# Performance work log

Measured on AMD Instinct MI355X. Metric: run time of the kernel, lower is better.

The kernel has to match this reference:

```python
import jax, jax.numpy as jnp
import numpy as np

B = 8192
H_IN = 128
H = 512
Z = 128
N = 512   # must equal H due to W_up(h,h) -> W_down(n,.) chaining in the source
RW = 16
TEMP = 0.666
EPS = 1e-20


def _xavier(key, shape):
    fan_in, fan_out = shape[0], shape[1]
    lim = float(np.sqrt(6.0 / (fan_in + fan_out)))
    return jax.random.uniform(key, shape, jnp.float32, -lim, lim)


def setup_inputs() -> dict:
    key = jax.random.key(0)
    ks = jax.random.split(key, 24)
    inp = {
        'latent': jax.random.normal(ks[0], (B, Z), jnp.float32),
        'inputs': jnp.zeros((B, H_IN), jnp.float32),
        'gumbel_u': jax.random.uniform(ks[1], (RW, B, N), jnp.float32),
        # weights stored [in, out] for x @ W
        'W_int': _xavier(ks[2], (Z, H)),   'b_int': jnp.zeros((H,), jnp.float32),
        'W_intl': _xavier(ks[3], (Z, H)),  'b_intl': jnp.zeros((H,), jnp.float32),
        'W_hup': _xavier(ks[4], (H, H)),   'b_hup': jnp.zeros((H,), jnp.float32),
        'W_cup': _xavier(ks[5], (H, H)),   'b_cup': jnp.zeros((H,), jnp.float32),
        'W_hupl': _xavier(ks[6], (H, H)),  'b_hupl': jnp.zeros((H,), jnp.float32),
        'W_cupl': _xavier(ks[7], (H, H)),  'b_cupl': jnp.zeros((H,), jnp.float32),
        'W_lstm': _xavier(ks[8], (H_IN + H, 4 * H)), 'b_lstm': jnp.zeros((4 * H,), jnp.float32),
        'W_up': _xavier(ks[9], (H, H)),    'b_up': jnp.zeros((H,), jnp.float32),
        'W_down': _xavier(ks[10], (N, H_IN)),        # no bias
        'W_downl': _xavier(ks[11], (N, H_IN)),       # no bias
        'W_outl': _xavier(ks[12], (H, 1)), 'b_outl': jnp.zeros((1,), jnp.float32),
    }
    return inp


def _lstm_step(x, hx, cx, W_lstm, b_lstm):
    gates = jnp.concatenate([x, hx], axis=1) @ W_lstm + b_lstm  # [B, 4H]
    i, g, f, o = jnp.split(gates, 4, axis=1)
    cy = cx * jax.nn.sigmoid(f + 1.0) + jax.nn.sigmoid(i) * jnp.tanh(g)
    hy = jax.nn.sigmoid(o) * jnp.tanh(cy)
    return hy, cy


def _forward(latent, inputs, gumbel_u,
             W_int, b_int, W_intl, b_intl,
             W_hup, b_hup, W_cup, b_cup,
             W_hupl, b_hupl, W_cupl, b_cupl,
             W_lstm, b_lstm, W_up, b_up,
             W_down, W_downl, W_outl, b_outl):
    inter = jnp.tanh(latent @ W_int + b_int)
    hx = jnp.tanh(inter @ W_hup + b_hup)
    cx = jnp.tanh(inter @ W_cup + b_cup)
    inter_l = jnp.tanh(latent @ W_intl + b_intl)
    hxl = jnp.tanh(inter_l @ W_hupl + b_hupl)
    cxl = jnp.tanh(inter_l @ W_cupl + b_cupl)

    def step1(carry, u):
        x, h, c = carry
        hy, cy = _lstm_step(x, h, c, W_lstm, b_lstm)
        logits = hy @ W_up + b_up                       # [B, N]
        g = -jnp.log(-jnp.log(u + EPS) + EPS)           # gumbel noise
        y = jax.nn.softmax((logits + g) / TEMP, axis=1)
        y_hard = (y == jnp.max(y, axis=1, keepdims=True)).astype(y.dtype)
        y = jax.lax.stop_gradient(y_hard - y) + y       # straight-through hard sample
        return (y @ W_down, hy, cy), y

    _, out_steps = jax.lax.scan(step1, (inputs, hx, cx), gumbel_u)  # [RW, B, N]

    def step2(carry, y):
        h, c = carry
        xl = y @ W_downl
        hy, cy = _lstm_step(xl, h, c, W_lstm, b_lstm)   # source reuses lstm_cell here
        return (hy, cy), hy @ W_outl + b_outl           # [B, 1]

    _, line_steps = jax.lax.scan(step2, (hxl, cxl), out_steps)      # [RW, B, 1]

    return (jnp.transpose(out_steps, (1, 0, 2)),   # [B, RW, N]
            jnp.transpose(line_steps, (1, 0, 2)))  # [B, RW, 1]


def reference(latent, inputs, gumbel_u,
              W_int, b_int, W_intl, b_intl,
              W_hup, b_hup, W_cup, b_cup,
              W_hupl, b_hupl, W_cupl, b_cupl,
              W_lstm, b_lstm, W_up, b_up,
              W_down, W_downl, W_outl, b_outl):
    return _forward(latent, inputs, gumbel_u,
                    W_int, b_int, W_intl, b_intl,
                    W_hup, b_hup, W_cup, b_cup,
                    W_hupl, b_hupl, W_cupl, b_cupl,
                    W_lstm, b_lstm, W_up, b_up,
                    W_down, W_downl, W_outl, b_outl)
```

## Files before the change

kernel.cpp:

```cpp
#include <hip/hip_runtime.h>

#define NB 8192
#define NH 512
#define NZ 128
#define NIN 128
#define NN 512
#define NRW 16
#define NG 2048

typedef _Float16 f16;
typedef _Float16 f16x8 __attribute__((ext_vector_type(8)));
typedef float f32x4 __attribute__((ext_vector_type(4)));

#define LO_SCALE 2048.0f
#define LO_INV   (1.0f / 2048.0f)

__device__ __forceinline__ float sigm(float x) { return 1.0f / (1.0f + expf(-x)); }

__device__ __forceinline__ int oc_of(int c)
{
    return (((c >> 4) & 3) << 9) + ((c >> 6) << 4) + (c & 15);
}
__device__ __forceinline__ int cperm(int j)
{
    return (j & 15) | (((j >> 4) & 31) << 6) | (((j >> 9) & 3) << 4);
}

__device__ __forceinline__ void swz_xcd(int& bx, int& by)
{
    const int gx = gridDim.x;
    const int nwg = gx * gridDim.y;
    int lin = by * gx + bx;
    lin = (lin & 7) * (nwg >> 3) + (lin >> 3);
    const int sh = 31 - __clz(gx);
    bx = lin & (gx - 1);
    by = lin >> sh;
}

__device__ __forceinline__ void gload16(const f16* g, f16* l)
{
    __builtin_amdgcn_global_load_lds(
        (const __attribute__((address_space(1))) void*)g,
        (__attribute__((address_space(3))) void*)l, 16, 0, 0);
}

__device__ __forceinline__ int swz4(int row) { return (row & 3) ^ ((row >> 2) & 3); }

__device__ __forceinline__ void stage_tile(f16* tilebase, const f16* src,
                                           int rowbase, int K, int kb,
                                           int wid, int lane)
{
#pragma unroll
    for (int q = 0; q < 2; ++q) {
        const int iw = wid * 2 + q;
        const int chunk = (iw << 6) | lane;
        const int row = chunk >> 2;
        const int p = (chunk & 3) ^ swz4(row);
        const f16* g = src + (size_t)(rowbase + row) * K + kb + (p << 3);
        gload16(g, tilebase + (iw << 9));
    }
}

__device__ __forceinline__ f16x8 frag(const f16* tile, int row, int sl)
{
    return *(const f16x8*)(tile + row * 32 + ((sl ^ swz4(row)) << 3));
}

__device__ __forceinline__ void gemm_core(const f16* Ahi, const f16* Alo,
                                          const f16* Bhi, const f16* Blo,
                                          f16 (*sT)[4][128 * 32],
                                          int bm, int bn, int K,
                                          int wid, int lane, int wr, int wc,
                                          f32x4 (&accA)[4][4], f32x4 (&accB)[4][4])
{
    const int NT = K >> 5;
    stage_tile(sT[0][0], Ahi, bm, K, 0, wid, lane);
    stage_tile(sT[0][1], Alo, bm, K, 0, wid, lane);
    __builtin_amdgcn_sched_barrier(0);
    stage_tile(sT[0][2], Bhi, bn, K, 0, wid, lane);
    __builtin_amdgcn_sched_barrier(0);
    stage_tile(sT[0][3], Blo, bn, K, 0, wid, lane);

    const int r16 = lane & 15, sl = lane >> 4;

    for (int kt = 0; kt < NT; ++kt) {
        const int cur = kt & 1;
        const int nxt = cur ^ 1;
        const bool more = (kt + 1 < NT);
        const int kb = (kt + 1) << 5;

        asm volatile("s_waitcnt vmcnt(2)" ::: "memory");
        __builtin_amdgcn_s_barrier();
        __builtin_amdgcn_sched_barrier(0);
        if (more) {
            stage_tile(sT[nxt][0], Ahi, bm, K, kb, wid, lane);
            stage_tile(sT[nxt][1], Alo, bm, K, kb, wid, lane);
        }
        f16x8 ah[4], bh[4];
#pragma unroll
        for (int f = 0; f < 4; ++f) {
            ah[f] = frag(sT[cur][0], wr + f * 16 + r16, sl);
            bh[f] = frag(sT[cur][2], wc + f * 16 + r16, sl);
        }
        __builtin_amdgcn_s_setprio(1);
#pragma unroll
        for (int i = 0; i < 4; ++i)
#pragma unroll
            for (int j = 0; j < 4; ++j)
                accA[i][j] = __builtin_amdgcn_mfma_f32_16x16x32_f16(ah[i], bh[j], accA[i][j], 0, 0, 0);
        __builtin_amdgcn_s_setprio(0);

        __builtin_amdgcn_s_barrier();
        __builtin_amdgcn_sched_barrier(0);
        if (more) stage_tile(sT[nxt][2], Bhi, bn, K, kb, wid, lane);
        f16x8 al[4];
#pragma unroll
        for (int f = 0; f < 4; ++f) al[f] = frag(sT[cur][1], wr + f * 16 + r16, sl);
        __builtin_amdgcn_s_setprio(1);
#pragma unroll
        for (int i = 0; i < 4; ++i)
#pragma unroll
            for (int j = 0; j < 4; ++j)
                accB[i][j] = __builtin_amdgcn_mfma_f32_16x16x32_f16(al[i], bh[j], accB[i][j], 0, 0, 0);
        __builtin_amdgcn_s_setprio(0);

        if (more) asm volatile("s_waitcnt vmcnt(6)" ::: "memory");
        else      asm volatile("s_waitcnt vmcnt(0)" ::: "memory");
        __builtin_amdgcn_s_barrier();
        __builtin_amdgcn_sched_barrier(0);
        if (more) stage_tile(sT[nxt][3], Blo, bn, K, kb, wid, lane);
        f16x8 bl[4];
#pragma unroll
        for (int f = 0; f < 4; ++f) bl[f] = frag(sT[cur][3], wc + f * 16 + r16, sl);
        __builtin_amdgcn_s_setprio(1);
#pragma unroll
        for (int i = 0; i < 4; ++i)
#pragma unroll
            for (int j = 0; j < 4; ++j)
                accB[i][j] = __builtin_amdgcn_mfma_f32_16x16x32_f16(ah[i], bl[j], accB[i][j], 0, 0, 0);
        __builtin_amdgcn_s_setprio(0);
    }
}

__device__ __forceinline__ void gemm_core1(const f16* Ahi, const f16* Bhi,
                                           f16 (*sT)[2][128 * 32],
                                           int bm, int bn, int K,
                                           int wid, int lane, int wr, int wc,
                                           f32x4 (&acc)[4][4])
{
    const int NT = K >> 5;
    stage_tile(sT[0][0], Ahi, bm, K, 0, wid, lane);
    stage_tile(sT[0][1], Bhi, bn, K, 0, wid, lane);

    const int r16 = lane & 15, sl = lane >> 4;

    for (int kt = 0; kt < NT; ++kt) {
        const int cur = kt & 1;
        const int nxt = cur ^ 1;
        __syncthreads();
        if (kt + 1 < NT) {
            const int kb = (kt + 1) << 5;
            stage_tile(sT[nxt][0], Ahi, bm, K, kb, wid, lane);
            stage_tile(sT[nxt][1], Bhi, bn, K, kb, wid, lane);
        }
        f16x8 ah[4], bh[4];
#pragma unroll
        for (int f = 0; f < 4; ++f) {
            ah[f] = frag(sT[cur][0], wr + f * 16 + r16, sl);
            bh[f] = frag(sT[cur][1], wc + f * 16 + r16, sl);
        }
        __builtin_amdgcn_s_setprio(1);
#pragma unroll
        for (int i = 0; i < 4; ++i)
#pragma unroll
            for (int j = 0; j < 4; ++j)
                acc[i][j] = __builtin_amdgcn_mfma_f32_16x16x32_f16(ah[i], bh[j], acc[i][j], 0, 0, 0);
        __builtin_amdgcn_s_setprio(0);
    }
}

template<int OUT>
__global__ __launch_bounds__(256, 2)
void mfma_gemm(const f16* __restrict__ Ahi, const f16* __restrict__ Alo,
               const f16* __restrict__ Bhi, const f16* __restrict__ Blo,
               const float* __restrict__ bias,
               float* __restrict__ C, f16* __restrict__ Ohi, f16* __restrict__ Olo,
               int N, int K)
{
    __shared__ f16 sT[2][4][128 * 32];
    int bx = blockIdx.x, by = blockIdx.y;
    swz_xcd(bx, by);
    const int bm = by << 7;
    const int bn = bx << 7;
    const int tid = threadIdx.x;
    const int wid = tid >> 6, lane = tid & 63;
    const int wr = ((wid >> 1) & 1) << 6;
    const int wc = (wid & 1) << 6;

    f32x4 accA[4][4], accB[4][4];
#pragma unroll
    for (int i = 0; i < 4; ++i)
#pragma unroll
        for (int j = 0; j < 4; ++j) { accA[i][j] = (f32x4)(0.0f); accB[i][j] = (f32x4)(0.0f); }

    gemm_core(Ahi, Alo, Bhi, Blo, sT, bm, bn, K, wid, lane, wr, wc, accA, accB);

    const int r16 = lane & 15;
    const int rg = lane >> 4;
#pragma unroll
    for (int i = 0; i < 4; ++i) {
#pragma unroll
        for (int r = 0; r < 4; ++r) {
            const int row = bm + wr + i * 16 + rg * 4 + r;
#pragma unroll
            for (int j = 0; j < 4; ++j) {
                const int col = bn + wc + j * 16 + r16;
                float v = accA[i][j][r] + accB[i][j][r] * LO_INV;
                if (bias) v += bias[col];
                if (OUT >= 1) v = tanhf(v);
                const size_t idx = (size_t)row * N + col;
                if (OUT <= 1) C[idx] = v;
                else {
                    const f16 a = (f16)v;
                    Ohi[idx] = a;
                    if (OUT == 2) Olo[idx] = (f16)((v - (float)a) * LO_SCALE);
                }
            }
        }
    }
}

__global__ __launch_bounds__(256, 2)
void mfma_logits_argmax(const f16* __restrict__ Ahi, const f16* __restrict__ Alo,
                        const f16* __restrict__ Bhi, const f16* __restrict__ Blo,
                        const float* __restrict__ bias,
                        const float* __restrict__ gu,
                        float2* __restrict__ part, int t)
{
    __shared__ f16 sT[2][4][128 * 32];
    int bx = blockIdx.x, by = blockIdx.y;
    swz_xcd(bx, by);
    const int bm = by << 7;
    const int bn = bx << 7;
    const int tid = threadIdx.x;
    const int wid = tid >> 6, lane = tid & 63;
    const int wr = ((wid >> 1) & 1) << 6;
    const int wc = (wid & 1) << 6;

    f32x4 accA[4][4], accB[4][4];
#pragma unroll
    for (int i = 0; i < 4; ++i)
#pragma unroll
        for (int j = 0; j < 4; ++j) { accA[i][j] = (f32x4)(0.0f); accB[i][j] = (f32x4)(0.0f); }

    gemm_core(Ahi, Alo, Bhi, Blo, sT, bm, bn, NN, wid, lane, wr, wc, accA, accB);

    const int r16 = lane & 15;
    const int rg = lane >> 4;
    const int cb = bx * 2 + (wc >> 6);
    float bi[4];
#pragma unroll
    for (int j = 0; j < 4; ++j) bi[j] = bias[bn + wc + j * 16 + r16];

#pragma unroll
    for (int i = 0; i < 4; ++i) {
#pragma unroll
        for (int r = 0; r < 4; ++r) {
            const int row = bm + wr + i * 16 + rg * 4 + r;
            const float* urow = gu + ((size_t)t * NB + row) * NN;
            float best = -INFINITY;
            int bidx = 0x7fffffff;
#pragma unroll
            for (int j = 0; j < 4; ++j) {
                const int col = bn + wc + j * 16 + r16;
                const float u = urow[col];
                const float g = -logf(-logf(u + 1e-20f) + 1e-20f);
                const float v = accA[i][j][r] + accB[i][j][r] * LO_INV + bi[j] + g;
                if (v > best || (v == best && col < bidx)) { best = v; bidx = col; }
            }
#pragma unroll
            for (int msk = 1; msk < 16; msk <<= 1) {
                const float ov = __shfl_xor(best, msk);
                const int oi = __shfl_xor(bidx, msk);
                if (ov > best || (ov == best && oi < bidx)) { best = ov; bidx = oi; }
            }
            if (r16 == 0) part[(size_t)row * 8 + cb] = make_float2(best, (float)bidx);
        }
    }
}

__global__ __launch_bounds__(256)
void finalize_argmax(const float2* __restrict__ part,
                     float* __restrict__ out0, int* __restrict__ kidx, int t)
{
    const int w = threadIdx.x >> 6;
    const int lane = threadIdx.x & 63;
    const int row = blockIdx.x * 4 + w;
    float best = -INFINITY;
    int bi = 0x7fffffff;
    if (lane < 8) {
        const float2 p = part[(size_t)row * 8 + lane];
        best = p.x;
        bi = (int)p.y;
    }
#pragma unroll
    for (int msk = 1; msk < 8; msk <<= 1) {
        const float ov = __shfl_xor(best, msk);
        const int oi = __shfl_xor(bi, msk);
        if (ov > best || (ov == best && oi < bi)) { best = ov; bi = oi; }
    }
    const int win = __shfl(bi, 0);
    if (lane == 0) kidx[(size_t)t * NB + row] = win;
    float* orow = out0 + ((size_t)row * NRW + t) * NN;
    const int c0 = lane * 8;
    float4 v0 = make_float4(c0 == win, c0 + 1 == win, c0 + 2 == win, c0 + 3 == win);
    float4 v1 = make_float4(c0 + 4 == win, c0 + 5 == win, c0 + 6 == win, c0 + 7 == win);
    *(float4*)(orow + c0) = v0;
    *(float4*)(orow + c0 + 4) = v1;
}

template<int HAS_EXTRA>
__global__ __launch_bounds__(256, 2)
void mfma_gate_lstm(const f16* __restrict__ Ahi, const f16* __restrict__ Alo,
                    const f16* __restrict__ Bhi, const f16* __restrict__ Blo,
                    const float* __restrict__ blp,
                    const float* __restrict__ extra, const int* __restrict__ eidx,
                    float* __restrict__ c,
                    f16* __restrict__ h_hi, f16* __restrict__ h_lo)
{
    __shared__ f16 sT[2][4][128 * 32];
    int bx = blockIdx.x, by = blockIdx.y;
    swz_xcd(bx, by);
    const int bm = by << 7;
    const int bn = bx << 7;
    const int tid = threadIdx.x;
    const int wid = tid >> 6, lane = tid & 63;
    const int wr = ((wid >> 1) & 1) << 6;
    const int wc = (wid & 1) << 6;

    f32x4 accA[4][4], accB[4][4];
#pragma unroll
    for (int i = 0; i < 4; ++i)
#pragma unroll
        for (int j = 0; j < 4; ++j) { accA[i][j] = (f32x4)(0.0f); accB[i][j] = (f32x4)(0.0f); }

    gemm_core(Ahi, Alo, Bhi, Blo, sT, bm, bn, NH, wid, lane, wr, wc, accA, accB);

    const int m = lane & 15;
    const int rg = lane >> 4;
    const int colb = bn + wc;
    const int jj = ((colb >> 6) << 4) + m;
    float bi[4];
#pragma unroll
    for (int g = 0; g < 4; ++g) bi[g] = blp[colb + g * 16 + m];

#pragma unroll
    for (int i = 0; i < 4; ++i) {
#pragma unroll
        for (int r = 0; r < 4; ++r) {
            const int row = bm + wr + i * 16 + rg * 4 + r;
            float ex[4] = {0.f, 0.f, 0.f, 0.f};
            if (HAS_EXTRA) {
                const float* exr = extra + (size_t)eidx[row] * NG;
#pragma unroll
                for (int g = 0; g < 4; ++g) ex[g] = exr[colb + g * 16 + m];
            }
            const float ig = accA[i][0][r] + accB[i][0][r] * LO_INV + bi[0] + ex[0];
            const float gg = accA[i][1][r] + accB[i][1][r] * LO_INV + bi[1] + ex[1];
            const float fg = accA[i][2][r] + accB[i][2][r] * LO_INV + bi[2] + ex[2];
            const float og = accA[i][3][r] + accB[i][3][r] * LO_INV + bi[3] + ex[3];
            const size_t cidx = (size_t)row * NH + jj;
            const float cx = c[cidx];
            const float cy = cx * sigm(fg + 1.0f) + sigm(ig) * tanhf(gg);
            const float hy = sigm(og) * tanhf(cy);
            c[cidx] = cy;
            const f16 a = (f16)hy;
            h_hi[cidx] = a;
            h_lo[cidx] = (f16)((hy - (float)a) * LO_SCALE);
        }
    }
}

__global__ __launch_bounds__(256, 2)
void mfma_gate_lstm2(const f16* __restrict__ Ahi, const f16* __restrict__ Bhi,
                     const float* __restrict__ blp,
                     const float* __restrict__ extra, const int* __restrict__ eidx,
                     float* __restrict__ c,
                     f16* __restrict__ h_hi,
                     const float* __restrict__ Woutl,
                     float* __restrict__ out1, int t)
{
    __shared__ f16 sT[2][2][128 * 32];
    int bx = blockIdx.x, by = blockIdx.y;
    swz_xcd(bx, by);
    const int bm = by << 7;
    const int bn = bx << 7;
    const int tid = threadIdx.x;
    const int wid = tid >> 6, lane = tid & 63;
    const int wr = ((wid >> 1) & 1) << 6;
    const int wc = (wid & 1) << 6;

    f32x4 acc[4][4];
#pragma unroll
    for (int i = 0; i < 4; ++i)
#pragma unroll
        for (int j = 0; j < 4; ++j) acc[i][j] = (f32x4)(0.0f);

    gemm_core1(Ahi, Bhi, sT, bm, bn, NH, wid, lane, wr, wc, acc);

    const int m = lane & 15;
    const int rg = lane >> 4;
    const int colb = bn + wc;
    const int jj = ((colb >> 6) << 4) + m;
    const float wout = Woutl[jj];
    float bi[4];
#pragma unroll
    for (int g = 0; g < 4; ++g) bi[g] = blp[colb + g * 16 + m];

#pragma unroll
    for (int i = 0; i < 4; ++i) {
#pragma unroll
        for (int r = 0; r < 4; ++r) {
            const int row = bm + wr + i * 16 + rg * 4 + r;
            const float* exr = extra + (size_t)eidx[row] * NG;
            float ex[4];
#pragma unroll
            for (int g = 0; g < 4; ++g) ex[g] = exr[colb + g * 16 + m];
            const float ig = acc[i][0][r] + bi[0] + ex[0];
            const float gg = acc[i][1][r] + bi[1] + ex[1];
            const float fg = acc[i][2][r] + bi[2] + ex[2];
            const float og = acc[i][3][r] + bi[3] + ex[3];
            const size_t cidx = (size_t)row * NH + jj;
            const float cx = c[cidx];
            const float cy = cx * sigm(fg + 1.0f) + sigm(ig) * tanhf(gg);
            const float hy = sigm(og) * tanhf(cy);
            c[cidx] = cy;
            h_hi[cidx] = (f16)hy;
            float part = hy * wout;
#pragma unroll
            for (int msk = 1; msk < 16; msk <<= 1) part += __shfl_xor(part, msk);
            if (m == 0) atomicAdd(&out1[(size_t)row * NRW + t], part);
        }
    }
}

__global__ __launch_bounds__(256)
void out1_init(float* __restrict__ out1, const float* __restrict__ boutl)
{
    const size_t i = (size_t)blockIdx.x * 256 + threadIdx.x;
    out1[i] = boutl[0];
}

template<int ACT, int PERM>
__global__ __launch_bounds__(256)
void gemm128(const float* __restrict__ A, int lda,
             const float* __restrict__ W, int ldw,
             const float* __restrict__ bias,
             float* __restrict__ C, int ldc, int K)
{
    __shared__ float As[16][128];
    __shared__ float Bs[16][128];
    const int bm = blockIdx.y << 7, bn = blockIdx.x << 7;
    const int tid = threadIdx.x;
    const int tx = tid & 15, ty = tid >> 4;
    const int sar = tid >> 1, sac = (tid & 1) << 3;
    const int sbk = tid >> 4, sbc = (tid & 15) << 3;
    float acc[2][2][4][4] = {};
    const float* Ap = A + (size_t)(bm + sar) * lda + sac;
    const float* Wp = W + (size_t)sbk * ldw + bn + sbc;
    for (int kb = 0; kb < K; kb += 16) {
        const float4 av0 = *(const float4*)(Ap + kb);
        const float4 av1 = *(const float4*)(Ap + kb + 4);
        const float4 bv0 = *(const float4*)(Wp + (size_t)kb * ldw);
        const float4 bv1 = *(const float4*)(Wp + (size_t)kb * ldw + 4);
// ... 19 lines not shown
#pragma unroll
                    for (int i = 0; i < 4; ++i)
#pragma unroll
                        for (int j = 0; j < 4; ++j)
                            acc[rh][ch][i][j] = fmaf(a[rh][i], b[ch][j], acc[rh][ch][i][j]);
        }
    }
    float4 bi4[2] = {make_float4(0.f, 0.f, 0.f, 0.f), make_float4(0.f, 0.f, 0.f, 0.f)};
    if (bias) {
        bi4[0] = *(const float4*)(bias + bn + (tx << 2));
        bi4[1] = *(const float4*)(bias + bn + 64 + (tx << 2));
    }
#pragma unroll
    for (int rh = 0; rh < 2; ++rh)
#pragma unroll
        for (int i = 0; i < 4; ++i) {
            const int row = bm + rh * 64 + (ty << 2) + i;
#pragma unroll
            for (int ch = 0; ch < 2; ++ch) {
                const int col = bn + ch * 64 + (tx << 2);
                float v0 = acc[rh][ch][i][0] + bi4[ch].x;
                float v1 = acc[rh][ch][i][1] + bi4[ch].y;
                float v2 = acc[rh][ch][i][2] + bi4[ch].z;
                float v3 = acc[rh][ch][i][3] + bi4[ch].w;
                if (ACT == 1) { v0 = tanhf(v0); v1 = tanhf(v1); v2 = tanhf(v2); v3 = tanhf(v3); }
                const int wcol = PERM ? cperm(col) : col;
                *(float4*)(C + (size_t)row * ldc + wcol) = make_float4(v0, v1, v2, v3);
            }
        }
}

template<int PERM>
__global__ __launch_bounds__(256)
void tsplit(const float* __restrict__ in, int ldin, int K,
            f16* __restrict__ ohi, f16* __restrict__ olo)
{
    __shared__ float t[32][33];
    const int kb = blockIdx.x << 5, nb = blockIdx.y << 5;
    const int cx = threadIdx.x & 31, ry = threadIdx.x >> 5;
    const int col = PERM ? oc_of(nb + cx) : (nb + cx);
#pragma unroll
    for (int q = 0; q < 4; ++q)
        t[ry + q * 8][cx] = in[(size_t)(kb + ry + q * 8) * ldin + col];
    __syncthreads();
#pragma unroll
    for (int q = 0; q < 4; ++q) {
        const int n = ry + q * 8;
        const float v = t[cx][n];
        const f16 hi = (f16)v;
        ohi[(size_t)(nb + n) * K + kb + cx] = hi;
        if (olo) olo[(size_t)(nb + n) * K + kb + cx] = (f16)((v - (float)hi) * LO_SCALE);
    }
}

__global__ __launch_bounds__(256)
void permb(const float* __restrict__ b, float* __restrict__ bp)
{
    const int c = blockIdx.x * 256 + threadIdx.x;
    bp[c] = b[oc_of(c)];
}

__global__ __launch_bounds__(256)
void split_h(const float* __restrict__ h, f16* __restrict__ hi, f16* __restrict__ lo)
{
    const size_t i = (size_t)blockIdx.x * 256 + threadIdx.x;
    const float v = h[i];
    const f16 a = (f16)v;
    hi[i] = a;
    lo[i] = (f16)((v - (float)a) * LO_SCALE);
}

extern "C" void kernel_launch(void* const* d_in, const int* in_sizes, int n_in,
                              void* d_out, int out_size, void* d_ws, size_t ws_size,
                              hipStream_t stream)
{
    const float* latent  = (const float*)d_in[0];
    const float* gu      = (const float*)d_in[2];
    const float* W_int   = (const float*)d_in[3];
    const float* b_int   = (const float*)d_in[4];
    const float* W_intl  = (const float*)d_in[5];
    const float* b_intl  = (const float*)d_in[6];
    const float* W_hup   = (const float*)d_in[7];
    const float* b_hup   = (const float*)d_in[8];
    const float* W_cup   = (const float*)d_in[9];
    const float* b_cup   = (const float*)d_in[10];
    const float* W_hupl  = (const float*)d_in[11];
    const float* b_hupl  = (const float*)d_in[12];
    const float* W_cupl  = (const float*)d_in[13];
    const float* b_cupl  = (const float*)d_in[14];
    const float* W_lstm  = (const float*)d_in[15];
    const float* b_lstm  = (const float*)d_in[16];
    const float* W_up    = (const float*)d_in[17];
    const float* b_up    = (const float*)d_in[18];
    const float* W_down  = (const float*)d_in[19];
    const float* W_downl = (const float*)d_in[20];
    const float* W_outl  = (const float*)d_in[21];
    const float* b_outl  = (const float*)d_in[22];

    float* out0 = (float*)d_out;
    float* out1 = out0 + (size_t)NB * NRW * NN;

    float* ws     = (float*)d_ws;
    float* c      = ws;
    float* logits = c + (size_t)NB * NH;
    float* gdown  = logits + (size_t)NB * NH;
    float* gdownl = gdown + (size_t)NN * NG;
    float* blp    = gdownl + (size_t)NN * NG;
    float2* part  = (float2*)(blp + NG);
    f16* fp = (f16*)(part + (size_t)NB * 8);
    f16* h_hi[2]; f16* h_lo[2];
    h_hi[0] = fp;                    fp += (size_t)NB * NH;
    h_lo[0] = fp;                    fp += (size_t)NB * NH;
    h_hi[1] = fp;                    fp += (size_t)NB * NH;
    h_lo[1] = fp;                    fp += (size_t)NB * NH;
    f16* i_hi   = fp;                fp += (size_t)NB * NH;
    f16* i_lo   = fp;                fp += (size_t)NB * NH;
    f16* WlT_hi = fp;                fp += (size_t)NG * NH;
    f16* WlT_lo = fp;                fp += (size_t)NG * NH;
    f16* WupT_hi = fp;               fp += (size_t)NN * NH;
    f16* WupT_lo = fp;               fp += (size_t)NN * NH;
    f16* WhT_hi = fp;                fp += (size_t)NH * NH;
    f16* WhT_lo = fp;                fp += (size_t)NH * NH;
    f16* WcT_hi = fp;                fp += (size_t)NH * NH;
    f16* WcT_lo = fp;                fp += (size_t)NH * NH;
    f16* WhlT_hi = fp;               fp += (size_t)NH * NH;
    f16* WhlT_lo = fp;               fp += (size_t)NH * NH;
    f16* WclT_hi = fp;               fp += (size_t)NH * NH;
    f16* WclT_lo = fp;               fp += (size_t)NH * NH;
    int* kidx = (int*)fp;

    const dim3 blk(256);
    const dim3 g_gates(NG / 128, NB / 128);
    const dim3 g_h(NH / 128, NB / 128);
    const dim3 g_pre(NG / 128, NN / 128);
    const dim3 g_sph(NB * NH / 256);

    tsplit<1><<<dim3(NH / 32, NG / 32), blk, 0, stream>>>(W_lstm + (size_t)NIN * NG, NG, NH, WlT_hi, WlT_lo);
    tsplit<0><<<dim3(NH / 32, NN / 32), blk, 0, stream>>>(W_up, NH, NH, WupT_hi, WupT_lo);
    tsplit<0><<<dim3(NH / 32, NH / 32), blk, 0, stream>>>(W_hup, NH, NH, WhT_hi, WhT_lo);
    tsplit<0><<<dim3(NH / 32, NH / 32), blk, 0, stream>>>(W_cup, NH, NH, WcT_hi, WcT_lo);
    tsplit<0><<<dim3(NH / 32, NH / 32), blk, 0, stream>>>(W_hupl, NH, NH, WhlT_hi, WhlT_lo);
    tsplit<0><<<dim3(NH / 32, NH / 32), blk, 0, stream>>>(W_cupl, NH, NH, WclT_hi, WclT_lo);
    permb<<<dim3(NG / 256), blk, 0, stream>>>(b_lstm, blp);
    gemm128<0, 1><<<g_pre, blk, 0, stream>>>(W_down, NIN, W_lstm, NG, nullptr, gdown, NG, NIN);
    gemm128<0, 1><<<g_pre, blk, 0, stream>>>(W_downl, NIN, W_lstm, NG, nullptr, gdownl, NG, NIN);

    gemm128<1, 0><<<g_h, blk, 0, stream>>>(latent, NZ, W_int, NH, b_int, logits, NH, NZ);
    split_h<<<g_sph, blk, 0, stream>>>(logits, i_hi, i_lo);
    mfma_gemm<2><<<g_h, blk, 0, stream>>>(i_hi, i_lo, WhT_hi, WhT_lo, b_hup,
                                          nullptr, h_hi[0], h_lo[0], NH, NH);
    mfma_gemm<1><<<g_h, blk, 0, stream>>>(i_hi, i_lo, WcT_hi, WcT_lo, b_cup,
                                          c, nullptr, nullptr, NH, NH);

    int cur = 0;
    for (int t = 0; t < NRW; ++t) {
        const int nxt = cur ^ 1;
        if (t == 0)
            mfma_gate_lstm<0><<<g_gates, blk, 0, stream>>>(h_hi[cur], h_lo[cur], WlT_hi, WlT_lo,
                                                           blp, nullptr, nullptr,
                                                           c, h_hi[nxt], h_lo[nxt]);
        else
            mfma_gate_lstm<1><<<g_gates, blk, 0, stream>>>(h_hi[cur], h_lo[cur], WlT_hi, WlT_lo,
                                                           blp, gdown, kidx + (size_t)(t - 1) * NB,
                                                           c, h_hi[nxt], h_lo[nxt]);
        mfma_logits_argmax<<<g_h, blk, 0, stream>>>(h_hi[nxt], h_lo[nxt], WupT_hi, WupT_lo,
                                                    b_up, gu, part, t);
        finalize_argmax<<<dim3(NB / 4), blk, 0, stream>>>(part, out0, kidx, t);
        cur = nxt;
    }

    gemm128<1, 0><<<g_h, blk, 0, stream>>>(latent, NZ, W_intl, NH, b_intl, logits, NH, NZ);
    split_h<<<g_sph, blk, 0, stream>>>(logits, i_hi, i_lo);
    mfma_gemm<3><<<g_h, blk, 0, stream>>>(i_hi, i_lo, WhlT_hi, WhlT_lo, b_hupl,
                                          nullptr, h_hi[0], nullptr, NH, NH);
    mfma_gemm<1><<<g_h, blk, 0, stream>>>(i_hi, i_lo, WclT_hi, WclT_lo, b_cupl,
                                          c, nullptr, nullptr, NH, NH);
    out1_init<<<dim3(NB * NRW / 256), blk, 0, stream>>>(out1, b_outl);

    cur = 0;
    for (int t = 0; t < NRW; ++t) {
        const int nxt = cur ^ 1;
        mfma_gate_lstm2<<<g_gates, blk, 0, stream>>>(h_hi[cur], WlT_hi,
                                                     blp, gdownl, kidx + (size_t)t * NB,
                                                     c, h_hi[nxt],
                                                     W_outl, out1, t);
        cur = nxt;
    }
}
```

Measured before the change: 3.088 ms.

## Pre-pack weights into MFMA fragment order and load B directly to registers

Weights are repacked by a new tsplit_pack kernel into per-fragment blocks so each wave loads its B operand straight from global memory into registers, and only the activation tile A is staged through LDS. The three split-precision products now go into a single accumulator without the 2048 lo-scale factor. The per-step finalize_argmax launch is folded into the next gate kernel, which reduces the partial maxima itself. This cuts LDS traffic, barriers and kernel launches per step, but B register loads bypass LDS reuse across waves, and dropping the lo scaling may cost precision through f16 underflow of the residual terms.

```diff
diff --git a/kernel.cpp b/kernel.cpp
--- a/kernel.cpp
+++ b/kernel.cpp
@@ -12,9 +12,6 @@
 typedef _Float16 f16x8 __attribute__((ext_vector_type(8)));
 typedef float f32x4 __attribute__((ext_vector_type(4)));
 
-#define LO_SCALE 2048.0f
-#define LO_INV   (1.0f / 2048.0f)
-
 __device__ __forceinline__ float sigm(float x) { return 1.0f / (1.0f + expf(-x)); }
 
 __device__ __forceinline__ int oc_of(int c)
@@ -47,8 +44,7 @@
 __device__ __forceinline__ int swz4(int row) { return (row & 3) ^ ((row >> 2) & 3); }
 
 __device__ __forceinline__ void stage_tile(f16* tilebase, const f16* src,
-                                           int rowbase, int K, int kb,
-                                           int wid, int lane)
+                                           int rowbase, int kb, int wid, int lane)
 {
 #pragma unroll
     for (int q = 0; q < 2; ++q) {
@@ -56,7 +52,7 @@
         const int chunk = (iw << 6) | lane;
         const int row = chunk >> 2;
         const int p = (chunk & 3) ^ swz4(row);
-        const f16* g = src + (size_t)(rowbase + row) * K + kb + (p << 3);
+        const f16* g = src + (size_t)(rowbase + row) * NH + kb + (p << 3);
         gload16(g, tilebase + (iw << 9));
     }
 }
@@ -66,115 +62,85 @@
     return *(const f16x8*)(tile + row * 32 + ((sl ^ swz4(row)) << 3));
 }
 
-__device__ __forceinline__ void gemm_core(const f16* Ahi, const f16* Alo,
-                                          const f16* Bhi, const f16* Blo,
-                                          f16 (*sT)[4][128 * 32],
-                                          int bm, int bn, int K,
-                                          int wid, int lane, int wr, int wc,
-                                          f32x4 (&accA)[4][4], f32x4 (&accB)[4][4])
-{
-    const int NT = K >> 5;
-    stage_tile(sT[0][0], Ahi, bm, K, 0, wid, lane);
-    stage_tile(sT[0][1], Alo, bm, K, 0, wid, lane);
-    __builtin_amdgcn_sched_barrier(0);
-    stage_tile(sT[0][2], Bhi, bn, K, 0, wid, lane);
-    __builtin_amdgcn_sched_barrier(0);
-    stage_tile(sT[0][3], Blo, bn, K, 0, wid, lane);
-
+__device__ __forceinline__ void readA(f16x8 (&a)[4], const f16* sbuf, int wr, int r16, int sl)
+{
+#pragma unroll
+    for (int f = 0; f < 4; ++f) a[f] = frag(sbuf, wr + f * 16 + r16, sl);
+}
+
+__device__ __forceinline__ void loadBfr(f16x8 (&d)[4], const f16* p, size_t base)
+{
+#pragma unroll
+    for (int f = 0; f < 4; ++f) d[f] = *(const f16x8*)(p + base + f * 512);
+}
+
+__device__ __forceinline__ f32x4 MM(const f16x8 a, const f16x8 b, f32x4 c)
+{
+    return __builtin_amdgcn_mfma_f32_16x16x32_f16(a, b, c, 0, 0, 0);
+}
+
+template<int SPLIT>
+__device__ __forceinline__ void core3(const f16* Ahi, const f16* Alo,
+                                      const f16* Bph, const f16* Bpl,
+                                      f16* s0h, f16* s0l, f16* s1h, f16* s1l,
+                                      int bm, int bnblk, int wid, int lane, int wr, int wc2,
+                                      f32x4 (&acc)[4][4])
+{
     const int r16 = lane & 15, sl = lane >> 4;
-
-    for (int kt = 0; kt < NT; ++kt) {
-        const int cur = kt & 1;
-        const int nxt = cur ^ 1;
-        const bool more = (kt + 1 < NT);
-        const int kb = (kt + 1) << 5;
-
-        asm volatile("s_waitcnt vmcnt(2)" ::: "memory");
-        __builtin_amdgcn_s_barrier();
-        __builtin_amdgcn_sched_barrier(0);
-        if (more) {
-            stage_tile(sT[nxt][0], Ahi, bm, K, kb, wid, lane);
-            stage_tile(sT[nxt][1], Alo, bm, K, kb, wid, lane);
-        }
-        f16x8 ah[4], bh[4];
-#pragma unroll
-        for (int f = 0; f < 4; ++f) {
-            ah[f] = frag(sT[cur][0], wr + f * 16 + r16, sl);
-            bh[f] = frag(sT[cur][2], wc + f * 16 + r16, sl);
-        }
+    const size_t bwoff = (size_t)(wc2 << 11) + lane * 8;
+    f16x8 bAh[4], bAl[4], bBh[4], bBl[4];
+
+    stage_tile(s0h, Ahi, bm, 0, wid, lane);
+    if (SPLIT) stage_tile(s0l, Alo, bm, 0, wid, lane);
+    loadBfr(bAh, Bph, (((size_t)bnblk << 4) << 12) + bwoff);
+    if (SPLIT) loadBfr(bAl, Bpl, (((size_t)bnblk << 4) << 12) + bwoff);
+
+#pragma unroll 1
+    for (int kt = 0; kt < 16; kt += 2) {
+        __syncthreads();
+        {
+            const int kn = kt + 1;
+            stage_tile(s1h, Ahi, bm, kn << 5, wid, lane);
+            if (SPLIT) stage_tile(s1l, Alo, bm, kn << 5, wid, lane);
+            loadBfr(bBh, Bph, ((((size_t)bnblk << 4) + kn) << 12) + bwoff);
+            if (SPLIT) loadBfr(bBl, Bpl, ((((size_t)bnblk << 4) + kn) << 12) + bwoff);
+        }
+        f16x8 ah[4], al[4];
+        readA(ah, s0h, wr, r16, sl);
+        if (SPLIT) readA(al, s0l, wr, r16, sl);
         __builtin_amdgcn_s_setprio(1);
 #pragma unroll
         for (int i = 0; i < 4; ++i)
 #pragma unroll
-            for (int j = 0; j < 4; ++j)
-                accA[i][j] = __builtin_amdgcn_mfma_f32_16x16x32_f16(ah[i], bh[j], accA[i][j], 0, 0, 0);
+            for (int j = 0; j < 4; ++j) {
+                acc[i][j] = MM(ah[i], bAh[j], acc[i][j]);
+                if (SPLIT) {
+                    acc[i][j] = MM(al[i], bAh[j], acc[i][j]);
+                    acc[i][j] = MM(ah[i], bAl[j], acc[i][j]);
+                }
+            }
         __builtin_amdgcn_s_setprio(0);
-
-        __builtin_amdgcn_s_barrier();
-        __builtin_amdgcn_sched_barrier(0);
-        if (more) stage_tile(sT[nxt][2], Bhi, bn, K, kb, wid, lane);
-        f16x8 al[4];
-#pragma unroll
-        for (int f = 0; f < 4; ++f) al[f] = frag(sT[cur][1], wr + f * 16 + r16, sl);
+        __syncthreads();
+        if (kt + 2 < 16) {
+            const int kn = kt + 2;
+            stage_tile(s0h, Ahi, bm, kn << 5, wid, lane);
+            if (SPLIT) stage_tile(s0l, Alo, bm, kn << 5, wid, lane);
+            loadBfr(bAh, Bph, ((((size_t)bnblk << 4) + kn) << 12) + bwoff);
+            if (SPLIT) loadBfr(bAl, Bpl, ((((size_t)bnblk << 4) + kn) << 12) + bwoff);
+        }
+        readA(ah, s1h, wr, r16, sl);
+        if (SPLIT) readA(al, s1l, wr, r16, sl);
         __builtin_amdgcn_s_setprio(1);
 #pragma unroll
         for (int i = 0; i < 4; ++i)
 #pragma unroll
-            for (int j = 0; j < 4; ++j)
-                accB[i][j] = __builtin_amdgcn_mfma_f32_16x16x32_f16(al[i], bh[j], accB[i][j], 0, 0, 0);
-        __builtin_amdgcn_s_setprio(0);
-
-        if (more) asm volatile("s_waitcnt vmcnt(6)" ::: "memory");
-        else      asm volatile("s_waitcnt vmcnt(0)" ::: "memory");
-        __builtin_amdgcn_s_barrier();
-        __builtin_amdgcn_sched_barrier(0);
-        if (more) stage_tile(sT[nxt][3], Blo, bn, K, kb, wid, lane);
-        f16x8 bl[4];
-#pragma unroll
-        for (int f = 0; f < 4; ++f) bl[f] = frag(sT[cur][3], wc + f * 16 + r16, sl);
-        __builtin_amdgcn_s_setprio(1);
-#pragma unroll
-        for (int i = 0; i < 4; ++i)
-#pragma unroll
-            for (int j = 0; j < 4; ++j)
-                accB[i][j] = __builtin_amdgcn_mfma_f32_16x16x32_f16(ah[i], bl[j], accB[i][j], 0, 0, 0);
-        __builtin_amdgcn_s_setprio(0);
-    }
-}
-
-__device__ __forceinline__ void gemm_core1(const f16* Ahi, const f16* Bhi,
-                                           f16 (*sT)[2][128 * 32],
-                                           int bm, int bn, int K,
-                                           int wid, int lane, int wr, int wc,
-                                           f32x4 (&acc)[4][4])
-{
-    const int NT = K >> 5;
-    stage_tile(sT[0][0], Ahi, bm, K, 0, wid, lane);
-    stage_tile(sT[0][1], Bhi, bn, K, 0, wid, lane);
-
-    const int r16 = lane & 15, sl = lane >> 4;
-
-    for (int kt = 0; kt < NT; ++kt) {
-        const int cur = kt & 1;
-        const int nxt = cur ^ 1;
-        __syncthreads();
-        if (kt + 1 < NT) {
-            const int kb = (kt + 1) << 5;
-            stage_tile(sT[nxt][0], Ahi, bm, K, kb, wid, lane);
-            stage_tile(sT[nxt][1], Bhi, bn, K, kb, wid, lane);
-        }
-        f16x8 ah[4], bh[4];
-#pragma unroll
-        for (int f = 0; f < 4; ++f) {
-            ah[f] = frag(sT[cur][0], wr + f * 16 + r16, sl);
-            bh[f] = frag(sT[cur][1], wc + f * 16 + r16, sl);
-        }
-        __builtin_amdgcn_s_setprio(1);
-#pragma unroll
-        for (int i = 0; i < 4; ++i)
-#pragma unroll
-            for (int j = 0; j < 4; ++j)
-                acc[i][j] = __builtin_amdgcn_mfma_f32_16x16x32_f16(ah[i], bh[j], acc[i][j], 0, 0, 0);
+            for (int j = 0; j < 4; ++j) {
+                acc[i][j] = MM(ah[i], bBh[j], acc[i][j]);
+                if (SPLIT) {
+                    acc[i][j] = MM(al[i], bBh[j], acc[i][j]);
+                    acc[i][j] = MM(ah[i], bBl[j], acc[i][j]);
+                }
+            }
         __builtin_amdgcn_s_setprio(0);
     }
 }
@@ -182,31 +148,28 @@
 template<int OUT>
 __global__ __launch_bounds__(256, 2)
 void mfma_gemm(const f16* __restrict__ Ahi, const f16* __restrict__ Alo,
-               const f16* __restrict__ Bhi, const f16* __restrict__ Blo,
+               const f16* __restrict__ Bph, const f16* __restrict__ Bpl,
                const float* __restrict__ bias,
-               float* __restrict__ C, f16* __restrict__ Ohi, f16* __restrict__ Olo,
-               int N, int K)
-{
-    __shared__ f16 sT[2][4][128 * 32];
+               float* __restrict__ C, f16* __restrict__ Ohi, f16* __restrict__ Olo)
+{
+    __shared__ f16 s[4][4096];
     int bx = blockIdx.x, by = blockIdx.y;
     swz_xcd(bx, by);
     const int bm = by << 7;
-    const int bn = bx << 7;
     const int tid = threadIdx.x;
     const int wid = tid >> 6, lane = tid & 63;
     const int wr = ((wid >> 1) & 1) << 6;
-    const int wc = (wid & 1) << 6;
-
-    f32x4 accA[4][4], accB[4][4];
+    const int wc2 = wid & 1;
+
+    f32x4 acc[4][4];
 #pragma unroll
     for (int i = 0; i < 4; ++i)
 #pragma unroll
-        for (int j = 0; j < 4; ++j) { accA[i][j] = (f32x4)(0.0f); accB[i][j] = (f32x4)(0.0f); }
-
-    gemm_core(Ahi, Alo, Bhi, Blo, sT, bm, bn, K, wid, lane, wr, wc, accA, accB);
-
-    const int r16 = lane & 15;
-    const int rg = lane >> 4;
+        for (int j = 0; j < 4; ++j) acc[i][j] = (f32x4)(0.0f);
+
+    core3<1>(Ahi, Alo, Bph, Bpl, s[0], s[1], s[2], s[3], bm, bx, wid, lane, wr, wc2, acc);
+
+    const int r16 = lane & 15, rg = lane >> 4;
 #pragma unroll
     for (int i = 0; i < 4; ++i) {
 #pragma unroll
@@ -214,16 +177,15 @@
             const int row = bm + wr + i * 16 + rg * 4 + r;
 #pragma unroll
             for (int j = 0; j < 4; ++j) {
-                const int col = bn + wc + j * 16 + r16;
-                float v = accA[i][j][r] + accB[i][j][r] * LO_INV;
-                if (bias) v += bias[col];
-                if (OUT >= 1) v = tanhf(v);
-                const size_t idx = (size_t)row * N + col;
-                if (OUT <= 1) C[idx] = v;
+                const int col = (bx << 7) + (wc2 << 6) + j * 16 + r16;
+                float v = acc[i][j][r] + bias[col];
+                v = tanhf(v);
+                const size_t idx = (size_t)row * NH + col;
+                if (OUT == 1) C[idx] = v;
                 else {
                     const f16 a = (f16)v;
                     Ohi[idx] = a;
-                    if (OUT == 2) Olo[idx] = (f16)((v - (float)a) * LO_SCALE);
+                    if (OUT == 2) Olo[idx] = (f16)(v - (float)a);
                 }
             }
         }
@@ -232,35 +194,33 @@
 
 __global__ __launch_bounds__(256, 2)
 void mfma_logits_argmax(const f16* __restrict__ Ahi, const f16* __restrict__ Alo,
-                        const f16* __restrict__ Bhi, const f16* __restrict__ Blo,
+                        const f16* __restrict__ Bph, const f16* __restrict__ Bpl,
                         const float* __restrict__ bias,
                         const float* __restrict__ gu,
                         float2* __restrict__ part, int t)
 {
-    __shared__ f16 sT[2][4][128 * 32];
+    __shared__ f16 s[4][4096];
     int bx = blockIdx.x, by = blockIdx.y;
     swz_xcd(bx, by);
     const int bm = by << 7;
-    const int bn = bx << 7;
     const int tid = threadIdx.x;
     const int wid = tid >> 6, lane = tid & 63;
     const int wr = ((wid >> 1) & 1) << 6;
-    const int wc = (wid & 1) << 6;
-
-    f32x4 accA[4][4], accB[4][4];
+    const int wc2 = wid & 1;
+
+    f32x4 acc[4][4];
 #pragma unroll
     for (int i = 0; i < 4; ++i)
 #pragma unroll
-        for (int j = 0; j < 4; ++j) { accA[i][j] = (f32x4)(0.0f); accB[i][j] = (f32x4)(0.0f); }
-
-    gemm_core(Ahi, Alo, Bhi, Blo, sT, bm, bn, NN, wid, lane, wr, wc, accA, accB);
-
-    const int r16 = lane & 15;
-    const int rg = lane >> 4;
-    const int cb = bx * 2 + (wc >> 6);
+        for (int j = 0; j < 4; ++j) acc[i][j] = (f32x4)(0.0f);
+
+    core3<1>(Ahi, Alo, Bph, Bpl, s[0], s[1], s[2], s[3], bm, bx, wid, lane, wr, wc2, acc);
+
+    const int r16 = lane & 15, rg = lane >> 4;
+    const int cb = (bx << 1) + wc2;
     float bi[4];
 #pragma unroll
-    for (int j = 0; j < 4; ++j) bi[j] = bias[bn + wc + j * 16 + r16];
+    for (int j = 0; j < 4; ++j) bi[j] = bias[(bx << 7) + (wc2 << 6) + j * 16 + r16];
 
 #pragma unroll
     for (int i = 0; i < 4; ++i) {
@@ -272,10 +232,10 @@
             int bidx = 0x7fffffff;
 #pragma unroll
             for (int j = 0; j < 4; ++j) {
-                const int col = bn + wc + j * 16 + r16;
+                const int col = (bx << 7) + (wc2 << 6) + j * 16 + r16;
                 const float u = urow[col];
                 const float g = -logf(-logf(u + 1e-20f) + 1e-20f);
-                const float v = accA[i][j][r] + accB[i][j][r] * LO_INV + bi[j] + g;
+                const float v = acc[i][j][r] + bi[j] + g;
                 if (v > best || (v == best && col < bidx)) { best = v; bidx = col; }
             }
 #pragma unroll
@@ -313,46 +273,58 @@
     if (lane == 0) kidx[(size_t)t * NB + row] = win;
     float* orow = out0 + ((size_t)row * NRW + t) * NN;
     const int c0 = lane * 8;
-    float4 v0 = make_float4(c0 == win, c0 + 1 == win, c0 + 2 == win, c0 + 3 == win);
-    float4 v1 = make_float4(c0 + 4 == win, c0 + 5 == win, c0 + 6 == win, c0 + 7 == win);
-    *(float4*)(orow + c0) = v0;
-    *(float4*)(orow + c0 + 4) = v1;
-}
-
-template<int HAS_EXTRA>
+    *(float4*)(orow + c0) = make_float4(c0 == win, c0 + 1 == win, c0 + 2 == win, c0 + 3 == win);
+    *(float4*)(orow + c0 + 4) = make_float4(c0 + 4 == win, c0 + 5 == win, c0 + 6 == win, c0 + 7 == win);
+}
+
+template<int HAS_PART>
 __global__ __launch_bounds__(256, 2)
 void mfma_gate_lstm(const f16* __restrict__ Ahi, const f16* __restrict__ Alo,
-                    const f16* __restrict__ Bhi, const f16* __restrict__ Blo,
+                    const f16* __restrict__ Bph, const f16* __restrict__ Bpl,
                     const float* __restrict__ blp,
-                    const float* __restrict__ extra, const int* __restrict__ eidx,
+                    const float* __restrict__ extra,
+                    const float2* __restrict__ part,
+                    int* __restrict__ kidx, float* __restrict__ out0, int t,
                     float* __restrict__ c,
                     f16* __restrict__ h_hi, f16* __restrict__ h_lo)
 {
-    __shared__ f16 sT[2][4][128 * 32];
+    __shared__ f16 s[4][4096];
+    __shared__ int winlds[128];
     int bx = blockIdx.x, by = blockIdx.y;
     swz_xcd(bx, by);
     const int bm = by << 7;
-    const int bn = bx << 7;
     const int tid = threadIdx.x;
     const int wid = tid >> 6, lane = tid & 63;
     const int wr = ((wid >> 1) & 1) << 6;
-    const int wc = (wid & 1) << 6;
-
-    f32x4 accA[4][4], accB[4][4];
+    const int wc2 = wid & 1;
+
+    if (HAS_PART && tid < 128) {
+        const float2* p = part + (size_t)(bm + tid) * 8;
+        float best = -INFINITY;
+        int bi = 0x7fffffff;
+#pragma unroll
+        for (int q = 0; q < 8; ++q) {
+            const float2 pv = p[q];
+            if (pv.x > best || (pv.x == best && (int)pv.y < bi)) { best = pv.x; bi = (int)pv.y; }
+        }
+        winlds[tid] = bi;
+        if (bx == 0) kidx[(size_t)(t - 1) * NB + bm + tid] = bi;
+    }
+
+    f32x4 acc[4][4];
 #pragma unroll
     for (int i = 0; i < 4; ++i)
 #pragma unroll
-        for (int j = 0; j < 4; ++j) { accA[i][j] = (f32x4)(0.0f); accB[i][j] = (f32x4)(0.0f); }
-
-    gemm_core(Ahi, Alo, Bhi, Blo, sT, bm, bn, NH, wid, lane, wr, wc, accA, accB);
-
-    const int m = lane & 15;
-    const int rg = lane >> 4;
-    const int colb = bn + wc;
+        for (int j = 0; j < 4; ++j) acc[i][j] = (f32x4)(0.0f);
+
+    core3<1>(Ahi, Alo, Bph, Bpl, s[0], s[1], s[2], s[3], bm, bx, wid, lane, wr, wc2, acc);
+
+    const int m = lane & 15, rg = lane >> 4;
+    const int colb = (bx << 7) + (wc2 << 6);
     const int jj = ((colb >> 6) << 4) + m;
-    float bi[4];
-#pragma unroll
-    for (int g = 0; g < 4; ++g) bi[g] = blp[colb + g * 16 + m];
+    float bi4[4];
+#pragma unroll
+    for (int g = 0; g < 4; ++g) bi4[g] = blp[colb + g * 16 + m];
 
 #pragma unroll
     for (int i = 0; i < 4; ++i) {
@@ -360,15 +332,15 @@
         for (int r = 0; r < 4; ++r) {
             const int row = bm + wr + i * 16 + rg * 4 + r;
             float ex[4] = {0.f, 0.f, 0.f, 0.f};
-            if (HAS_EXTRA) {
-                const float* exr = extra + (size_t)eidx[row] * NG;
+            if (HAS_PART) {
+                const float* exr = extra + (size_t)winlds[row - bm] * NG;
 #pragma unroll
                 for (int g = 0; g < 4; ++g) ex[g] = exr[colb + g * 16 + m];
             }
-            const float ig = accA[i][0][r] + accB[i][0][r] * LO_INV + bi[0] + ex[0];
-            const float gg = accA[i][1][r] + accB[i][1][r] * LO_INV + bi[1] + ex[1];
-            const float fg = accA[i][2][r] + accB[i][2][r] * LO_INV + bi[2] + ex[2];
-            const float og = accA[i][3][r] + accB[i][3][r] * LO_INV + bi[3] + ex[3];
+            const float ig = acc[i][0][r] + bi4[0] + ex[0];
+            const float gg = acc[i][1][r] + bi4[1] + ex[1];
+            const float fg = acc[i][2][r] + bi4[2] + ex[2];
+            const float og = acc[i][3][r] + bi4[3] + ex[3];
             const size_t cidx = (size_t)row * NH + jj;
             const float cx = c[cidx];
             const float cy = cx * sigm(fg + 1.0f) + sigm(ig) * tanhf(gg);
@@ -376,13 +348,25 @@
             c[cidx] = cy;
             const f16 a = (f16)hy;
             h_hi[cidx] = a;
-            h_lo[cidx] = (f16)((hy - (float)a) * LO_SCALE);
-        }
-    }
-}
-
-__global__ __launch_bounds__(256, 2)
-void mfma_gate_lstm2(const f16* __restrict__ Ahi, const f16* __restrict__ Bhi,
+            h_lo[cidx] = (f16)(hy - (float)a);
+        }
+    }
+
+    if (HAS_PART) {
+        const int rr = tid >> 1;
+        const int cs = (bx << 5) + ((tid & 1) << 4);
+        const int win = winlds[rr];
+        float* orow = out0 + ((size_t)(bm + rr) * NRW + (t - 1)) * NN + cs;
+#pragma unroll
+        for (int e = 0; e < 16; e += 4) {
+            const int c0 = cs + e;
+            *(float4*)(orow + e) = make_float4(c0 == win, c0 + 1 == win, c0 + 2 == win, c0 + 3 == win);
+        }
+    }
+}
+
+__global__ __launch_bounds__(256, 3)
+void mfma_gate_lstm2(const f16* __restrict__ Ahi, const f16* __restrict__ Bph,
                      const float* __restrict__ blp,
                      const float* __restrict__ extra, const int* __restrict__ eidx,
                      float* __restrict__ c,
@@ -390,15 +374,14 @@
                      const float* __restrict__ Woutl,
                      float* __restrict__ out1, int t)
 {
-    __shared__ f16 sT[2][2][128 * 32];
+    __shared__ f16 s[2][4096];
     int bx = blockIdx.x, by = blockIdx.y;
     swz_xcd(bx, by);
     const int bm = by << 7;
-    const int bn = bx << 7;
     const int tid = threadIdx.x;
     const int wid = tid >> 6, lane = tid & 63;
     const int wr = ((wid >> 1) & 1) << 6;
-    const int wc = (wid & 1) << 6;
+    const int wc2 = wid & 1;
 
     f32x4 acc[4][4];
 #pragma unroll
@@ -406,16 +389,16 @@
 #pragma unroll
         for (int j = 0; j < 4; ++j) acc[i][j] = (f32x4)(0.0f);
 
-    gemm_core1(Ahi, Bhi, sT, bm, bn, NH, wid, lane, wr, wc, acc);
-
-    const int m = lane & 15;
-    const int rg = lane >> 4;
-    const int colb = bn + wc;
+    core3<0>(Ahi, nullptr, Bph, nullptr, s[0], nullptr, s[1], nullptr,
+             bm, bx, wid, lane, wr, wc2, acc);
+
+    const int m = lane & 15, rg = lane >> 4;
+    const int colb = (bx << 7) + (wc2 << 6);
     const int jj = ((colb >> 6) << 4) + m;
     const float wout = Woutl[jj];
-    float bi[4];
-#pragma unroll
-    for (int g = 0; g < 4; ++g) bi[g] = blp[colb + g * 16 + m];
+    float bi4[4];
+#pragma unroll
+    for (int g = 0; g < 4; ++g) bi4[g] = blp[colb + g * 16 + m];
 
 #pragma unroll
     for (int i = 0; i < 4; ++i) {
@@ -426,20 +409,20 @@
             float ex[4];
 #pragma unroll
             for (int g = 0; g < 4; ++g) ex[g] = exr[colb + g * 16 + m];
-            const float ig = acc[i][0][r] + bi[0] + ex[0];
-            const float gg = acc[i][1][r] + bi[1] + ex[1];
-            const float fg = acc[i][2][r] + bi[2] + ex[2];
-            const float og = acc[i][3][r] + bi[3] + ex[3];
+            const float ig = acc[i][0][r] + bi4[0] + ex[0];
+            const float gg = acc[i][1][r] + bi4[1] + ex[1];
+            const float fg = acc[i][2][r] + bi4[2] + ex[2];
+            const float og = acc[i][3][r] + bi4[3] + ex[3];
             const size_t cidx = (size_t)row * NH + jj;
             const float cx = c[cidx];
             const float cy = cx * sigm(fg + 1.0f) + sigm(ig) * tanhf(gg);
             const float hy = sigm(og) * tanhf(cy);
             c[cidx] = cy;
             h_hi[cidx] = (f16)hy;
-            float part = hy * wout;
-#pragma unroll
-            for (int msk = 1; msk < 16; msk <<= 1) part += __shfl_xor(part, msk);
-            if (m == 0) atomicAdd(&out1[(size_t)row * NRW + t], part);
+            float pt = hy * wout;
+#pragma unroll
+            for (int msk = 1; msk < 16; msk <<= 1) pt += __shfl_xor(pt, msk);
+            if (m == 0) atomicAdd(&out1[(size_t)row * NRW + t], pt);
         }
     }
 }
@@ -525,24 +508,29 @@
 
 template<int PERM>
 __global__ __launch_bounds__(256)
-void tsplit(const float* __restrict__ in, int ldin, int K,
-            f16* __restrict__ ohi, f16* __restrict__ olo)
-{
-    __shared__ float t[32][33];
-    const int kb = blockIdx.x << 5, nb = blockIdx.y << 5;
-    const int cx = threadIdx.x & 31, ry = threadIdx.x >> 5;
-    const int col = PERM ? oc_of(nb + cx) : (nb + cx);
-#pragma unroll
-    for (int q = 0; q < 4; ++q)
-        t[ry + q * 8][cx] = in[(size_t)(kb + ry + q * 8) * ldin + col];
-    __syncthreads();
-#pragma unroll
-    for (int q = 0; q < 4; ++q) {
-        const int n = ry + q * 8;
-        const float v = t[cx][n];
-        const f16 hi = (f16)v;
-        ohi[(size_t)(nb + n) * K + kb + cx] = hi;
-        if (olo) olo[(size_t)(nb + n) * K + kb + cx] = (f16)((v - (float)hi) * LO_SCALE);
+void tsplit_pack(const float* __restrict__ in, int ldin,
+                 f16* __restrict__ phi, f16* __restrict__ plo)
+{
+    const int kt = blockIdx.x;
+    const int nblk = blockIdx.y;
+#pragma unroll
+    for (int q = 0; q < 2; ++q) {
+        const int cch = threadIdx.x + q * 256;
+        const int wc2 = cch >> 8, f = (cch >> 6) & 3, slc = (cch >> 4) & 3, r16 = cch & 15;
+        const int n = (nblk << 7) + (wc2 << 6) + (f << 4) + r16;
+        const int ncol = PERM ? oc_of(n) : n;
+        const int k0 = (kt << 5) + (slc << 3);
+        f16x8 h8, l8;
+#pragma unroll
+        for (int e = 0; e < 8; ++e) {
+            const float v = in[(size_t)(k0 + e) * ldin + ncol];
+            const f16 hi = (f16)v;
+            h8[e] = hi;
+            l8[e] = (f16)(v - (float)hi);
+        }
+        const size_t off = ((((size_t)nblk << 4) + kt) << 12) + (size_t)cch * 8;
+        *(f16x8*)(phi + off) = h8;
+        *(f16x8*)(plo + off) = l8;
     }
 }
 
@@ -560,7 +548,7 @@
     const float v = h[i];
     const f16 a = (f16)v;
     hi[i] = a;
-    lo[i] = (f16)((v - (float)a) * LO_SCALE);
+    lo[i] = (f16)(v - (float)a);
 }
 
 extern "C" void kernel_launch(void* const* d_in, const int* in_sizes, int n_in,
@@ -608,18 +596,18 @@
     h_lo[1] = fp;                    fp += (size_t)NB * NH;
     f16* i_hi   = fp;                fp += (size_t)NB * NH;
     f16* i_lo   = fp;                fp += (size_t)NB * NH;
-    f16* WlT_hi = fp;                fp += (size_t)NG * NH;
-    f16* WlT_lo = fp;                fp += (size_t)NG * NH;
-    f16* WupT_hi = fp;               fp += (size_t)NN * NH;
-    f16* WupT_lo = fp;               fp += (size_t)NN * NH;
-    f16* WhT_hi = fp;                fp += (size_t)NH * NH;
-    f16* WhT_lo = fp;                fp += (size_t)NH * NH;
-    f16* WcT_hi = fp;                fp += (size_t)NH * NH;
-    f16* WcT_lo = fp;                fp += (size_t)NH * NH;
-    f16* WhlT_hi = fp;               fp += (size_t)NH * NH;
-    f16* WhlT_lo = fp;               fp += (size_t)NH * NH;
-    f16* WclT_hi = fp;               fp += (size_t)NH * NH;
-    f16* WclT_lo = fp;               fp += (size_t)NH * NH;
+    f16* Wlp_hi = fp;                fp += (size_t)NG * NH;
+    f16* Wlp_lo = fp;                fp += (size_t)NG * NH;
+    f16* Wup_hi = fp;                fp += (size_t)NN * NH;
+    f16* Wup_lo = fp;                fp += (size_t)NN * NH;
+    f16* Whp_hi = fp;                fp += (size_t)NH * NH;
+    f16* Whp_lo = fp;                fp += (size_t)NH * NH;
+    f16* Wcp_hi = fp;                fp += (size_t)NH * NH;
+    f16* Wcp_lo = fp;                fp += (size_t)NH * NH;
+    f16* Whlp_hi = fp;               fp += (size_t)NH * NH;
+    f16* Whlp_lo = fp;               fp += (size_t)NH * NH;
+    f16* Wclp_hi = fp;               fp += (size_t)NH * NH;
+    f16* Wclp_lo = fp;               fp += (size_t)NH * NH;
     int* kidx = (int*)fp;
 
     const dim3 blk(256);
@@ -628,52 +616,52 @@
     const dim3 g_pre(NG / 128, NN / 128);
     const dim3 g_sph(NB * NH / 256);
 
-    tsplit<1><<<dim3(NH / 32, NG / 32), blk, 0, stream>>>(W_lstm + (size_t)NIN * NG, NG, NH, WlT_hi, WlT_lo);
-    tsplit<0><<<dim3(NH / 32, NN / 32), blk, 0, stream>>>(W_up, NH, NH, WupT_hi, WupT_lo);
-    tsplit<0><<<dim3(NH / 32, NH / 32), blk, 0, stream>>>(W_hup, NH, NH, WhT_hi, WhT_lo);
-    tsplit<0><<<dim3(NH / 32, NH / 32), blk, 0, stream>>>(W_cup, NH, NH, WcT_hi, WcT_lo);
-    tsplit<0><<<dim3(NH / 32, NH / 32), blk, 0, stream>>>(W_hupl, NH, NH, WhlT_hi, WhlT_lo);
-    tsplit<0><<<dim3(NH / 32, NH / 32), blk, 0, stream>>>(W_cupl, NH, NH, WclT_hi, WclT_lo);
+    tsplit_pack<1><<<dim3(16, NG / 128), blk, 0, stream>>>(W_lstm + (size_t)NIN * NG, NG, Wlp_hi, Wlp_lo);
+    tsplit_pack<0><<<dim3(16, NN / 128), blk, 0, stream>>>(W_up, NH, Wup_hi, Wup_lo);
+    tsplit_pack<0><<<dim3(16, NH / 128), blk, 0, stream>>>(W_hup, NH, Whp_hi, Whp_lo);
+    tsplit_pack<0><<<dim3(16, NH / 128), blk, 0, stream>>>(W_cup, NH, Wcp_hi, Wcp_lo);
+    tsplit_pack<0><<<dim3(16, NH / 128), blk, 0, stream>>>(W_hupl, NH, Whlp_hi, Whlp_lo);
+    tsplit_pack<0><<<dim3(16, NH / 128), blk, 0, stream>>>(W_cupl, NH, Wclp_hi, Wclp_lo);
     permb<<<dim3(NG / 256), blk, 0, stream>>>(b_lstm, blp);
     gemm128<0, 1><<<g_pre, blk, 0, stream>>>(W_down, NIN, W_lstm, NG, nullptr, gdown, NG, NIN);
     gemm128<0, 1><<<g_pre, blk, 0, stream>>>(W_downl, NIN, W_lstm, NG, nullptr, gdownl, NG, NIN);
 
     gemm128<1, 0><<<g_h, blk, 0, stream>>>(latent, NZ, W_int, NH, b_int, logits, NH, NZ);
     split_h<<<g_sph, blk, 0, stream>>>(logits, i_hi, i_lo);
-    mfma_gemm<2><<<g_h, blk, 0, stream>>>(i_hi, i_lo, WhT_hi, WhT_lo, b_hup,
-                                          nullptr, h_hi[0], h_lo[0], NH, NH);
-    mfma_gemm<1><<<g_h, blk, 0, stream>>>(i_hi, i_lo, WcT_hi, WcT_lo, b_cup,
-                                          c, nullptr, nullptr, NH, NH);
+    mfma_gemm<2><<<g_h, blk, 0, stream>>>(i_hi, i_lo, Whp_hi, Whp_lo, b_hup,
+                                          nullptr, h_hi[0], h_lo[0]);
+    mfma_gemm<1><<<g_h, blk, 0, stream>>>(i_hi, i_lo, Wcp_hi, Wcp_lo, b_cup,
+                                          c, nullptr, nullptr);
 
     int cur = 0;
     for (int t = 0; t < NRW; ++t) {
         const int nxt = cur ^ 1;
         if (t == 0)
-            mfma_gate_lstm<0><<<g_gates, blk, 0, stream>>>(h_hi[cur], h_lo[cur], WlT_hi, WlT_lo,
-                                                           blp, nullptr, nullptr,
+            mfma_gate_lstm<0><<<g_gates, blk, 0, stream>>>(h_hi[cur], h_lo[cur], Wlp_hi, Wlp_lo,
+                                                           blp, nullptr, nullptr, nullptr, nullptr, t,
                                                            c, h_hi[nxt], h_lo[nxt]);
         else
-            mfma_gate_lstm<1><<<g_gates, blk, 0, stream>>>(h_hi[cur], h_lo[cur], WlT_hi, WlT_lo,
-                                                           blp, gdown, kidx + (size_t)(t - 1) * NB,
+            mfma_gate_lstm<1><<<g_gates, blk, 0, stream>>>(h_hi[cur], h_lo[cur], Wlp_hi, Wlp_lo,
+                                                           blp, gdown, part, kidx, out0, t,
                                                            c, h_hi[nxt], h_lo[nxt]);
-        mfma_logits_argmax<<<g_h, blk, 0, stream>>>(h_hi[nxt], h_lo[nxt], WupT_hi, WupT_lo,
+        mfma_logits_argmax<<<g_h, blk, 0, stream>>>(h_hi[nxt], h_lo[nxt], Wup_hi, Wup_lo,
                                                     b_up, gu, part, t);
-        finalize_argmax<<<dim3(NB / 4), blk, 0, stream>>>(part, out0, kidx, t);
         cur = nxt;
     }
+    finalize_argmax<<<dim3(NB / 4), blk, 0, stream>>>(part, out0, kidx, NRW - 1);
 
     gemm128<1, 0><<<g_h, blk, 0, stream>>>(latent, NZ, W_intl, NH, b_intl, logits, NH, NZ);
     split_h<<<g_sph, blk, 0, stream>>>(logits, i_hi, i_lo);
-    mfma_gemm<3><<<g_h, blk, 0, stream>>>(i_hi, i_lo, WhlT_hi, WhlT_lo, b_hupl,
-                                          nullptr, h_hi[0], nullptr, NH, NH);
-    mfma_gemm<1><<<g_h, blk, 0, stream>>>(i_hi, i_lo, WclT_hi, WclT_lo, b_cupl,
-                                          c, nullptr, nullptr, NH, NH);
+    mfma_gemm<3><<<g_h, blk, 0, stream>>>(i_hi, i_lo, Whlp_hi, Whlp_lo, b_hupl,
+                                          nullptr, h_hi[0], nullptr);
+    mfma_gemm<1><<<g_h, blk, 0, stream>>>(i_hi, i_lo, Wclp_hi, Wclp_lo, b_cupl,
+                                          c, nullptr, nullptr);
     out1_init<<<dim3(NB * NRW / 256), blk, 0, stream>>>(out1, b_outl);
 
     cur = 0;
     for (int t = 0; t < NRW; ++t) {
         const int nxt = cur ^ 1;
-        mfma_gate_lstm2<<<g_gates, blk, 0, stream>>>(h_hi[cur], WlT_hi,
+        mfma_gate_lstm2<<<g_gates, blk, 0, stream>>>(h_hi[cur], Wlp_hi,
                                                      blp, gdownl, kidx + (size_t)t * NB,
                                                      c, h_hi[nxt],
                                                      W_outl, out1, t);
```

New measurement: 2.882 ms. 6.7% less time.
